# Kernel optimization log

Hardware: AMD Instinct MI355X
Metric: run time of the kernel (lower is better)

The kernel has to match this reference:

```python
import jax, jax.numpy as jnp
import numpy as np

N_NODES = 50000
N_EDGES = 600000
D_IN = 128
D_HID = 128
N_CLASS = 40


def gcn_conv(x, edge_index, W, b, num_nodes):
    """PyG GCNConv: add self-loops, symmetric normalization, weight-then-propagate."""
    row, col = edge_index[0], edge_index[1]
    loop = jnp.arange(num_nodes)
    row = jnp.concatenate([row, loop])
    col = jnp.concatenate([col, loop])
    ew = jnp.ones(row.shape[0], dtype=x.dtype)
    deg = jax.ops.segment_sum(ew, col, num_segments=num_nodes)  # in-degree incl. self-loop
    dinv = jnp.where(deg > 0, jax.lax.rsqrt(deg), jnp.zeros((), x.dtype))
    norm = dinv[row] * dinv[col]  # [E+N]
    xw = x @ W  # [N, D]
    msg = norm[:, None] * xw[row]  # gather + scale, [E+N, D]
    out = jax.ops.segment_sum(msg, col, num_segments=num_nodes)  # scatter-add
    return out + b


def setup_inputs() -> dict:
    key = jax.random.key(0)
    ks = jax.random.split(key, 8)
    s_in = 1.0 / np.sqrt(D_IN)
    s_hid = 1.0 / np.sqrt(D_HID)
    return {
        "x": jax.random.normal(ks[0], (N_NODES, D_IN), jnp.float32),
        "edge_index": jax.random.randint(ks[1], (2, N_EDGES), 0, N_NODES, dtype=jnp.int64),
        "W_in": jax.random.normal(ks[2], (D_IN, D_HID), jnp.float32) * s_in,
        "b_in": jnp.zeros((D_HID,), jnp.float32),
        "W_gcn": jax.random.normal(ks[3], (D_HID, D_HID), jnp.float32) * s_hid,
        "b_gcn": jnp.zeros((D_HID,), jnp.float32),
        "W_cls": jax.random.normal(ks[4], (D_HID, N_CLASS), jnp.float32) * s_hid,
        "b_cls": jnp.zeros((N_CLASS,), jnp.float32),
    }


def reference(x, edge_index, W_in, b_in, W_gcn, b_gcn, W_cls, b_cls):
    h = jax.nn.relu(x @ W_in + b_in)               # linear_transform_in
    g = gcn_conv(h, edge_index, W_gcn, b_gcn, N_NODES)  # GCNConv
    y_hat = jax.nn.relu(g) @ W_cls + b_cls          # linear_cls_out
    return y_hat
```

## Files before the change

### kernel.cpp

```cpp
#include <hip/hip_runtime.h>


typedef __bf16 bf16x8 __attribute__((ext_vector_type(8)));
typedef float f32x4 __attribute__((ext_vector_type(4)));

#define NBUCK 512
#define CH_MAX 4704
#define PREP_BLKS 76
#define SCAP 1024

__device__ __forceinline__ ushort f2b(float f) {
  uint u = __float_as_uint(f);
  return (ushort)((u + 0x7FFFu + ((u >> 16) & 1u)) >> 16);
}
__device__ __forceinline__ float b2f_lo(uint u) { return __uint_as_float(u << 16); }
__device__ __forceinline__ float b2f_hi(uint u) { return __uint_as_float(u & 0xFFFF0000u); }

__device__ __forceinline__ void acc8s(float* a, uint4 v, float d) {
  a[0] = fmaf(d, b2f_lo(v.x), a[0]); a[1] = fmaf(d, b2f_hi(v.x), a[1]);
  a[2] = fmaf(d, b2f_lo(v.y), a[2]); a[3] = fmaf(d, b2f_hi(v.y), a[3]);
  a[4] = fmaf(d, b2f_lo(v.z), a[4]); a[5] = fmaf(d, b2f_hi(v.z), a[5]);
  a[6] = fmaf(d, b2f_lo(v.w), a[6]); a[7] = fmaf(d, b2f_hi(v.w), a[7]);
}

template<bool ABF16, bool RELU, bool BIAS>
__device__ __forceinline__ void gemm_tile_512(const void* __restrict__ Ap,
                                              const ushort* __restrict__ Wt,
                                              const float* __restrict__ bias,
                                              ushort* __restrict__ O,
                                              int nrows, int row0,
                                              char* smem, int tid) {
  ushort (*As)[136] = (ushort(*)[136])smem;
  ushort (*Bs)[136] = (ushort(*)[136])(smem + 128 * 136 * 2);
#pragma unroll
  for (int q = 0; q < 4; ++q) {
    int f = tid + 512 * q;
    int r = f >> 4, cw = f & 15;
    *(uint4*)&Bs[r][cw * 8] = *(const uint4*)&Wt[r * 128 + cw * 8];
  }
  if (ABF16) {
    const ushort* A = (const ushort*)Ap;
#pragma unroll
    for (int q = 0; q < 4; ++q) {
      int f = tid + 512 * q;
      int r = f >> 4, cw = f & 15;
      uint4 v = make_uint4(0u, 0u, 0u, 0u);
      if (row0 + r < nrows) v = *(const uint4*)&A[(size_t)(row0 + r) * 128 + cw * 8];
      *(uint4*)&As[r][cw * 8] = v;
    }
  } else {
    const float* A = (const float*)Ap;
#pragma unroll
    for (int q = 0; q < 8; ++q) {
      int f = tid + 512 * q;
      int r = f >> 5, kc = f & 31;
      float4 v = make_float4(0.f, 0.f, 0.f, 0.f);
      if (row0 + r < nrows) v = *(const float4*)&A[(size_t)(row0 + r) * 128 + kc * 4];
      ushort4 o;
      o.x = f2b(v.x); o.y = f2b(v.y); o.z = f2b(v.z); o.w = f2b(v.w);
      *(ushort4*)&As[r][kc * 4] = o;
    }
  }
  __syncthreads();

  const int wid = tid >> 6, lane = tid & 63;
  const int fr = lane & 15, fg = lane >> 4;
  f32x4 acc[8];
#pragma unroll
  for (int nn = 0; nn < 8; ++nn) acc[nn] = (f32x4){0.f, 0.f, 0.f, 0.f};
#pragma unroll
  for (int ks = 0; ks < 4; ++ks) {
    const int kb = ks * 32 + fg * 8;
    bf16x8 a = *(const bf16x8*)&As[wid * 16 + fr][kb];
#pragma unroll
    for (int nn = 0; nn < 8; ++nn) {
      bf16x8 b = *(const bf16x8*)&Bs[nn * 16 + fr][kb];
      acc[nn] = __builtin_amdgcn_mfma_f32_16x16x32_bf16(a, b, acc[nn], 0, 0, 0);
    }
  }
  const int r0 = row0 + wid * 16 + fg * 4;
#pragma unroll
  for (int nn = 0; nn < 8; ++nn) {
    const int cn = nn * 16 + fr;
    const float bv = BIAS ? bias[cn] : 0.f;
#pragma unroll
    for (int i = 0; i < 4; ++i) {
      const int rr = r0 + i;
      if (rr < nrows) {
        float v = acc[nn][i] + bv;
        if (RELU) v = fmaxf(v, 0.f);
        O[(size_t)rr * 128 + cn] = f2b(v);
      }
    }
  }
}

__global__ __launch_bounds__(512) void k_L1_prep_chist(const float* __restrict__ Wi,
                                                       const float* __restrict__ Wg,
                                                       const float* __restrict__ Wc,
                                                       ushort* __restrict__ Ti,
                                                       ushort* __restrict__ Tg,
                                                       ushort* __restrict__ Tc,
                                                       const int* __restrict__ col,
                                                       int* __restrict__ H2,
                                                       int E, int chunk, int sortb) {
  __shared__ int hist[NBUCK];
  const int tid = threadIdx.x;
  if (blockIdx.x < PREP_BLKS) {
    int idx = blockIdx.x * 512 + tid;
    if (idx < 16384) {
      int c = idx >> 7, k = idx & 127;
      Ti[c * 128 + k] = f2b(Wi[k * 128 + c]);
    } else if (idx < 32768) {
      int j = idx - 16384;
      int c = j >> 7, k = j & 127;
      Tg[c * 128 + k] = f2b(Wg[k * 128 + c]);
    } else if (idx < 38912) {
      int j = idx - 32768;
      int c = j >> 7, k = j & 127;
      Tc[c * 128 + k] = (c < 40) ? f2b(Wc[k * 40 + c]) : (ushort)0;
    }
    return;
  }
  const int blk = blockIdx.x - PREP_BLKS;
  if (tid < NBUCK) hist[tid] = 0;
  __syncthreads();
  const int e0 = blk * chunk;
  const int cnt = min(chunk, E - e0);
  for (int i = tid; i < cnt; i += 512)
    atomicAdd(&hist[((unsigned)col[e0 + i]) >> 7], 1);
  __syncthreads();
  if (tid < NBUCK) H2[tid * sortb + blk] = hist[tid];
}

__global__ __launch_bounds__(512) void k_L2_scan_g1a(const int* __restrict__ H2,
                                                     int* __restrict__ Hs,
                                                     int* __restrict__ cursor,
                                                     int sortb,
                                                     const float* __restrict__ x,
                                                     const ushort* __restrict__ Wti,
                                                     const float* __restrict__ b_in,
                                                     ushort* __restrict__ h, int nrows) {
  __shared__ __align__(16) char smem[69632];
  const int tid = threadIdx.x;
  if (blockIdx.x == 0) {
    int* sd = (int*)smem;
    int s = 0;
    const int4* p = (const int4*)&H2[tid * sortb];
    for (int j = 0; j < sortb / 4; ++j) { int4 v = p[j]; s += v.x + v.y + v.z + v.w; }
    sd[tid] = s;
    __syncthreads();
    for (int off = 1; off < 512; off <<= 1) {
      int u = (tid >= off) ? sd[tid - off] : 0;
      __syncthreads();
      sd[tid] += u;
      __syncthreads();
    }
    Hs[tid] = sd[tid] - s;
    if (tid == 511) Hs[NBUCK] = sd[511];
    cursor[tid] = 0;
    return;
  }
  gemm_tile_512<false, true, true>(x, Wti, b_in, h, nrows,
                                   (blockIdx.x - 1) * 128, smem, tid);
}

__global__ __launch_bounds__(512) void k_L3_reorder_g1b_g2a(const int* __restrict__ row,
                                                            const int* __restrict__ col,
                                                            const int* __restrict__ Hs,
                                                            int* __restrict__ cursor,
                                                            uint* __restrict__ ebuf,
                                                            int E, int chunk, int sortb,
                                                            const float* __restrict__ x,
                                                            const ushort* __restrict__ Wti,
                                                            const float* __restrict__ b_in,
                                                            const ushort* __restrict__ Wtg,
                                                            ushort* __restrict__ h,
                                                            ushort* __restrict__ xws,
                                                            int nrows) {
  __shared__ __align__(16) char smem[69632];
  const int tid = threadIdx.x;
  const int NT = (nrows + 127) >> 7;
  const int SPLIT = (NT + 1) >> 1;
  if (blockIdx.x < (unsigned)sortb) {
    int* hist   = (int*)smem;
    int* lstart = hist + NBUCK;
    int* cnt2   = lstart + NBUCK;
    int* obase  = cnt2 + NBUCK;
    uint* data  = (uint*)(obase + NBUCK);
    int* gpos   = (int*)(data + CH_MAX);
    int* sd     = gpos + CH_MAX;
    hist[tid] = 0; cnt2[tid] = 0;
    __syncthreads();
    const int e0 = blockIdx.x * chunk;
    const int cnt = min(chunk, E - e0);
    for (int i = tid; i < cnt; i += 512)
      atomicAdd(&hist[((unsigned)col[e0 + i]) >> 7], 1);
    __syncthreads();
    const int h0 = hist[tid];
    sd[tid] = h0;
    __syncthreads();
    for (int off = 1; off < 512; off <<= 1) {
      int u = (tid >= off) ? sd[tid - off] : 0;
      __syncthreads();
      sd[tid] += u;
      __syncthreads();
    }
    lstart[tid] = sd[tid] - h0;
    obase[tid] = Hs[tid] + (h0 ? atomicAdd(&cursor[tid], h0) : 0);
    __syncthreads();
    for (int i = tid; i < cnt; i += 512) {
      const int c = col[e0 + i], r = row[e0 + i];
      const int b = ((unsigned)c) >> 7;
      const int rk = atomicAdd(&cnt2[b], 1);
      const int slot = lstart[b] + rk;
      data[slot] = ((uint)(c & 127) << 16) | (uint)r;
      gpos[slot] = obase[b] + rk;
    }
    __syncthreads();
    for (int i = tid; i < cnt; i += 512)
      ebuf[gpos[i]] = data[i];
    return;
  }
  const int t = blockIdx.x - sortb;
  if (t < NT - SPLIT) {
    gemm_tile_512<false, true, true>(x, Wti, b_in, h, nrows,
                                     (SPLIT + t) * 128, smem, tid);
  } else {
    gemm_tile_512<true, false, false>(h, Wtg, nullptr, xws, nrows,
                                      (t - (NT - SPLIT)) * 128, smem, tid);
  }
}

__global__ __launch_bounds__(512) void k_L4_sort_g2b(const uint* __restrict__ ebuf,
                                                     const int* __restrict__ Hs,
                                                     int* __restrict__ srcrow,
                                                     int* __restrict__ P,
                                                     float* __restrict__ dinv,
                                                     int nbuck,
                                                     const ushort* __restrict__ h,
                                                     const ushort* __restrict__ Wtg,
                                                     ushort* __restrict__ xws,
                                                     int n) {
  __shared__ __align__(16) char smem[69632];
  const int tid = threadIdx.x;
  if (blockIdx.x < (unsigned)nbuck) {
    int* cnt    = (int*)smem;
    int* lstart = cnt + 128;
    int* cnt2   = lstart + 128;
    int* sd     = cnt2 + 128;
    if (tid < 128) { cnt[tid] = 0; cnt2[tid] = 0; }
    __syncthreads();
    const int b = blockIdx.x;
    const int start = Hs[b];
    const int end = Hs[b + 1];
    for (int i = start + tid; i < end; i += 512)
      atomicAdd(&cnt[ebuf[i] >> 16], 1);
    __syncthreads();
    const int cv = (tid < 128) ? cnt[tid] : 0;
    sd[tid] = cv;
    __syncthreads();
    for (int off = 1; off < 128; off <<= 1) {
      int u = (tid >= off) ? sd[tid - off] : 0;
      __syncthreads();
      sd[tid] += u;
      __syncthreads();
    }
    if (tid < 128) {
      const int ex = sd[tid] - cv;
      lstart[tid] = ex;
      const int node = b * 128 + tid;
      if (node < n) {
        P[node] = start + ex + cv;
        dinv[node] = rsqrtf((float)cv + 1.0f);
      }
    }
    __syncthreads();
    for (int i = start + tid; i < end; i += 512) {
      const uint v = ebuf[i];
      const int c = v >> 16;
      const int rk = atomicAdd(&cnt2[c], 1);
      srcrow[start + lstart[c] + rk] = (int)(v & 0xFFFFu);
    }
    return;
  }
  const int NT = (n + 127) >> 7;
  const int SPLIT = (NT + 1) >> 1;
  const int t = blockIdx.x - nbuck;
  gemm_tile_512<true, false, false>(h, Wtg, nullptr, xws, n,
                                    (SPLIT + t) * 128, smem, tid);
}

__global__ __launch_bounds__(512) void k_aggout(const int* __restrict__ P,
                                                const int* __restrict__ srcrow,
                                                const ushort* __restrict__ xws,
                                                const float* __restrict__ dinv,
                                                const float* __restrict__ b_gcn,
                                                const ushort* __restrict__ Wtc,
                                                const float* __restrict__ bc,
                                                float* __restrict__ out, int n) {
  __shared__ ushort ts[32][136];
  __shared__ ushort Bs[48][136];
  __shared__ int eLds[SCAP];
  __shared__ int pb[33];
  __shared__ int nextn;
  const int tid = threadIdx.x;
  const int row0 = blockIdx.x * 32;
#pragma unroll
  for (int q = 0; q < 2; ++q) {
    int f = tid + 512 * q;
    if (f < 768) {
      int r = f >> 4, cw = f & 15;
      *(uint4*)&Bs[r][cw * 8] = *(const uint4*)&Wtc[r * 128 + cw * 8];
    }
  }
  if (tid < 33) {
    int node = row0 + tid - 1;
    pb[tid] = (node < 0) ? 0 : P[node < n ? node : (n - 1)];
  }
  if (tid == 0) nextn = 0;
  __syncthreads();
  const int sStart = pb[0];
  const int tot = pb[32] - sStart;
  const bool inL = (tot <= SCAP);
  if (inL) {
    for (int i = tid; i < tot; i += 512) eLds[i] = srcrow[sStart + i];
  }
  __syncthreads();

  const int wid = tid >> 6, lane = tid & 63;
  const int qt = lane >> 4, lq = lane & 15;
  const size_t coff = (size_t)lq * 8;

  float bg[8];
#pragma unroll
  for (int j = 0; j < 8; ++j) bg[j] = b_gcn[lq * 8 + j];

  for (;;) {
    int idx;
    if (lane == 0) idx = atomicAdd(&nextn, 1);
    idx = __shfl(idx, 0);
    if (idx >= 32) break;
    const int c = row0 + idx;
    if (c < n) {
      const int len = pb[idx + 1] - pb[idx];
      float a[8];
#pragma unroll
      for (int j = 0; j < 8; ++j) a[j] = 0.f;
      if (inL) {
        const int base = pb[idx] - sStart;
        int e = 0;
        for (; e + 8 <= len; e += 8) {
          const int r0 = eLds[base + e + qt];
          const int r1 = eLds[base + e + 4 + qt];
          const float d0 = dinv[r0], d1 = dinv[r1];
          const uint4 v0 = *(const uint4*)&xws[(size_t)r0 * 128 + coff];
          const uint4 v1 = *(const uint4*)&xws[(size_t)r1 * 128 + coff];
          acc8s(a, v0, d0);
          acc8s(a, v1, d1);
        }
        for (; e < len; e += 4) {
          if (e + qt < len) {
            const int r = eLds[base + e + qt];
            const float d = dinv[r];
            const uint4 v = *(const uint4*)&xws[(size_t)r * 128 + coff];
            acc8s(a, v, d);
          }
        }
      } else {
        const int base = pb[idx];
        int e = 0;
        for (; e + 8 <= len; e += 8) {
          const int r0 = srcrow[base + e + qt];
          const int r1 = srcrow[base + e + 4 + qt];
          const float d0 = dinv[r0], d1 = dinv[r1];
          const uint4 v0 = *(const uint4*)&xws[(size_t)r0 * 128 + coff];
          const uint4 v1 = *(const uint4*)&xws[(size_t)r1 * 128 + coff];
          acc8s(a, v0, d0);
          acc8s(a, v1, d1);
        }
        for (; e < len; e += 4) {
          if (e + qt < len) {
            const int r = srcrow[base + e + qt];
            const float d = dinv[r];
            const uint4 v = *(const uint4*)&xws[(size_t)r * 128 + coff];
            acc8s(a, v, d);
          }
        }
      }
#pragma unroll
      for (int j = 0; j < 8; ++j) {
        a[j] += __shfl_xor(a[j], 16);
        a[j] += __shfl_xor(a[j], 32);
      }
      if (qt == 0) {
        const uint4 sv = *(const uint4*)&xws[(size_t)c * 128 + coff];
        const float dc = dinv[c];
        acc8s(a, sv, dc);
        const float t0 = fmaxf(fmaf(dc, a[0], bg[0]), 0.f);
        const float t1 = fmaxf(fmaf(dc, a[1], bg[1]), 0.f);
        const float t2 = fmaxf(fmaf(dc, a[2], bg[2]), 0.f);
        const float t3 = fmaxf(fmaf(dc, a[3], bg[3]), 0.f);
        const float t4 = fmaxf(fmaf(dc, a[4], bg[4]), 0.f);
        const float t5 = fmaxf(fmaf(dc, a[5], bg[5]), 0.f);
        const float t6 = fmaxf(fmaf(dc, a[6], bg[6]), 0.f);
        const float t7 = fmaxf(fmaf(dc, a[7], bg[7]), 0.f);
        uint4 o;
        o.x = ((uint)f2b(t1) << 16) | f2b(t0);
        o.y = ((uint)f2b(t3) << 16) | f2b(t2);
        o.z = ((uint)f2b(t5) << 16) | f2b(t4);
        o.w = ((uint)f2b(t7) << 16) | f2b(t6);
        *(uint4*)&ts[idx][coff] = o;
      }
    } else if (qt == 0) {
      *(uint4*)&ts[idx][coff] = make_uint4(0u, 0u, 0u, 0u);
    }
  }
  __syncthreads();

  if (wid < 6) {
    const int rb = wid & 1, nb = wid >> 1;
    const int fr = lane & 15, fg = lane >> 4;
    f32x4 acc = (f32x4){0.f, 0.f, 0.f, 0.f};
#pragma unroll
    for (int ks = 0; ks < 4; ++ks) {
      const int kb = ks * 32 + fg * 8;
      bf16x8 aa = *(const bf16x8*)&ts[rb * 16 + fr][kb];
      bf16x8 bb = *(const bf16x8*)&Bs[nb * 16 + fr][kb];
      acc = __builtin_amdgcn_mfma_f32_16x16x32_bf16(aa, bb, acc, 0, 0, 0);
    }
    const int cn = nb * 16 + fr;
    if (cn < 40) {
      const float bv = bc[cn];
      const int r0 = row0 + rb * 16 + fg * 4;
#pragma unroll
      for (int i = 0; i < 4; ++i) {
        const int rr = r0 + i;
        if (rr < n) out[(size_t)rr * 40 + cn] = acc[i] + bv;
      }
    }
  }
}

extern "C" void kernel_launch(void* const* d_in, const int* in_sizes, int n_in,
                              void* d_out, int out_size, void* d_ws, size_t ws_size,
                              hipStream_t stream) {
  const float* x     = (const float*)d_in[0];
  const int*   ei    = (const int*)d_in[1];
  const float* W_in  = (const float*)d_in[2];
  const float* b_in  = (const float*)d_in[3];
  const float* W_gcn = (const float*)d_in[4];
  const float* b_gcn = (const float*)d_in[5];
  const float* W_cls = (const float*)d_in[6];
  const float* b_cls = (const float*)d_in[7];
  float* out = (float*)d_out;

  const int N = in_sizes[0] / 128;
  const int E = in_sizes[1] / 2;
  const int* row = ei;
  const int* col = ei + E;

  const int sortb = (E + CH_MAX - 1) / CH_MAX;
  const int chunk = (E + sortb - 1) / sortb;
  const int nbuck = (N + 127) >> 7;
  const int NT    = (N + 127) >> 7;
  const int SPLIT = (NT + 1) >> 1;

  ushort* h      = (ushort*)d_ws;
  ushort* xws    = h + (size_t)N * 128;
  ushort* Wti    = xws + (size_t)N * 128;
  ushort* Wtg    = Wti + 128 * 128;
  ushort* Wtc    = Wtg + 128 * 128;
  uint*   ebuf   = (uint*)(Wtc + 48 * 128);
  int*    srcrow = (int*)(ebuf + E);
  int*    H2     = srcrow + E;
  int*    Hs     = H2 + NBUCK * sortb;
  int*    cursor = Hs + NBUCK + 1;
  int*    P      = cursor + NBUCK;
  float*  dinv   = (float*)(P + N);

  k_L1_prep_chist<<<PREP_BLKS + sortb, 512, 0, stream>>>(
      W_in, W_gcn, W_cls, Wti, Wtg, Wtc, col, H2, E, chunk, sortb);

  k_L2_scan_g1a<<<1 + SPLIT, 512, 0, stream>>>(
      H2, Hs, cursor, sortb, x, Wti, b_in, h, N);

  k_L3_reorder_g1b_g2a<<<sortb + (NT - SPLIT) + SPLIT, 512, 0, stream>>>(
      row, col, Hs, cursor, ebuf, E, chunk, sortb,
      x, Wti, b_in, Wtg, h, xws, N);

  k_L4_sort_g2b<<<nbuck + (NT - SPLIT), 512, 0, stream>>>(
      ebuf, Hs, srcrow, P, dinv, nbuck, h, Wtg, xws, N);

  k_aggout<<<(N + 31) / 32, 512, 0, stream>>>(
      P, srcrow, xws, dinv, b_gcn, Wtc, b_cls, out, N);
}
```

Baseline: 79.64 us.

## Fuse input linear and GCN weight GEMMs per tile, rebalance across kernels

```diff
diff --git a/kernel.cpp b/kernel.cpp
--- a/kernel.cpp
+++ b/kernel.cpp
@@ -23,43 +23,30 @@
   a[6] = fmaf(d, b2f_lo(v.w), a[6]); a[7] = fmaf(d, b2f_hi(v.w), a[7]);
 }
 
-template<bool ABF16, bool RELU, bool BIAS>
-__device__ __forceinline__ void gemm_tile_512(const void* __restrict__ Ap,
-                                              const ushort* __restrict__ Wt,
-                                              const float* __restrict__ bias,
-                                              ushort* __restrict__ O,
-                                              int nrows, int row0,
-                                              char* smem, int tid) {
+__device__ __forceinline__ void g12_tile_512(const float* __restrict__ x,
+                                             const ushort* __restrict__ Wti,
+                                             const ushort* __restrict__ Wtg,
+                                             const float* __restrict__ b_in,
+                                             ushort* __restrict__ xws,
+                                             int nrows, int row0,
+                                             char* smem, int tid) {
   ushort (*As)[136] = (ushort(*)[136])smem;
   ushort (*Bs)[136] = (ushort(*)[136])(smem + 128 * 136 * 2);
 #pragma unroll
   for (int q = 0; q < 4; ++q) {
     int f = tid + 512 * q;
     int r = f >> 4, cw = f & 15;
-    *(uint4*)&Bs[r][cw * 8] = *(const uint4*)&Wt[r * 128 + cw * 8];
-  }
-  if (ABF16) {
-    const ushort* A = (const ushort*)Ap;
-#pragma unroll
-    for (int q = 0; q < 4; ++q) {
-      int f = tid + 512 * q;
-      int r = f >> 4, cw = f & 15;
-      uint4 v = make_uint4(0u, 0u, 0u, 0u);
-      if (row0 + r < nrows) v = *(const uint4*)&A[(size_t)(row0 + r) * 128 + cw * 8];
-      *(uint4*)&As[r][cw * 8] = v;
-    }
-  } else {
-    const float* A = (const float*)Ap;
-#pragma unroll
-    for (int q = 0; q < 8; ++q) {
-      int f = tid + 512 * q;
-      int r = f >> 5, kc = f & 31;
-      float4 v = make_float4(0.f, 0.f, 0.f, 0.f);
-      if (row0 + r < nrows) v = *(const float4*)&A[(size_t)(row0 + r) * 128 + kc * 4];
-      ushort4 o;
-      o.x = f2b(v.x); o.y = f2b(v.y); o.z = f2b(v.z); o.w = f2b(v.w);
-      *(ushort4*)&As[r][kc * 4] = o;
-    }
+    *(uint4*)&Bs[r][cw * 8] = *(const uint4*)&Wti[r * 128 + cw * 8];
+  }
+#pragma unroll
+  for (int q = 0; q < 8; ++q) {
+    int f = tid + 512 * q;
+    int r = f >> 5, kc = f & 31;
+    float4 v = make_float4(0.f, 0.f, 0.f, 0.f);
+    if (row0 + r < nrows) v = *(const float4*)&x[(size_t)(row0 + r) * 128 + kc * 4];
+    ushort4 o;
+    o.x = f2b(v.x); o.y = f2b(v.y); o.z = f2b(v.z); o.w = f2b(v.w);
+    *(ushort4*)&As[r][kc * 4] = o;
   }
   __syncthreads();
 
@@ -78,19 +65,45 @@
       acc[nn] = __builtin_amdgcn_mfma_f32_16x16x32_bf16(a, b, acc[nn], 0, 0, 0);
     }
   }
-  const int r0 = row0 + wid * 16 + fg * 4;
+  __syncthreads();
+
 #pragma unroll
   for (int nn = 0; nn < 8; ++nn) {
     const int cn = nn * 16 + fr;
-    const float bv = BIAS ? bias[cn] : 0.f;
+    const float bv = b_in[cn];
+#pragma unroll
+    for (int i = 0; i < 4; ++i)
+      As[wid * 16 + fg * 4 + i][cn] = f2b(fmaxf(acc[nn][i] + bv, 0.f));
+  }
+#pragma unroll
+  for (int q = 0; q < 4; ++q) {
+    int f = tid + 512 * q;
+    int r = f >> 4, cw = f & 15;
+    *(uint4*)&Bs[r][cw * 8] = *(const uint4*)&Wtg[r * 128 + cw * 8];
+  }
+  __syncthreads();
+
+  f32x4 acc2[8];
+#pragma unroll
+  for (int nn = 0; nn < 8; ++nn) acc2[nn] = (f32x4){0.f, 0.f, 0.f, 0.f};
+#pragma unroll
+  for (int ks = 0; ks < 4; ++ks) {
+    const int kb = ks * 32 + fg * 8;
+    bf16x8 a = *(const bf16x8*)&As[wid * 16 + fr][kb];
+#pragma unroll
+    for (int nn = 0; nn < 8; ++nn) {
+      bf16x8 b = *(const bf16x8*)&Bs[nn * 16 + fr][kb];
+      acc2[nn] = __builtin_amdgcn_mfma_f32_16x16x32_bf16(a, b, acc2[nn], 0, 0, 0);
+    }
+  }
+  const int r0 = row0 + wid * 16 + fg * 4;
+#pragma unroll
+  for (int nn = 0; nn < 8; ++nn) {
+    const int cn = nn * 16 + fr;
 #pragma unroll
     for (int i = 0; i < 4; ++i) {
       const int rr = r0 + i;
-      if (rr < nrows) {
-        float v = acc[nn][i] + bv;
-        if (RELU) v = fmaxf(v, 0.f);
-        O[(size_t)rr * 128 + cn] = f2b(v);
-      }
+      if (rr < nrows) xws[(size_t)rr * 128 + cn] = f2b(acc2[nn][i]);
     }
   }
 }
@@ -133,14 +146,16 @@
   if (tid < NBUCK) H2[tid * sortb + blk] = hist[tid];
 }
 
-__global__ __launch_bounds__(512) void k_L2_scan_g1a(const int* __restrict__ H2,
+__global__ __launch_bounds__(512) void k_L2_scan_g12(const int* __restrict__ H2,
                                                      int* __restrict__ Hs,
                                                      int* __restrict__ cursor,
                                                      int sortb,
                                                      const float* __restrict__ x,
                                                      const ushort* __restrict__ Wti,
+                                                     const ushort* __restrict__ Wtg,
                                                      const float* __restrict__ b_in,
-                                                     ushort* __restrict__ h, int nrows) {
+                                                     ushort* __restrict__ xws,
+                                                     int nrows) {
   __shared__ __align__(16) char smem[69632];
   const int tid = threadIdx.x;
   if (blockIdx.x == 0) {
@@ -161,27 +176,23 @@
     cursor[tid] = 0;
     return;
   }
-  gemm_tile_512<false, true, true>(x, Wti, b_in, h, nrows,
-                                   (blockIdx.x - 1) * 128, smem, tid);
-}
-
-__global__ __launch_bounds__(512) void k_L3_reorder_g1b_g2a(const int* __restrict__ row,
-                                                            const int* __restrict__ col,
-                                                            const int* __restrict__ Hs,
-                                                            int* __restrict__ cursor,
-                                                            uint* __restrict__ ebuf,
-                                                            int E, int chunk, int sortb,
-                                                            const float* __restrict__ x,
-                                                            const ushort* __restrict__ Wti,
-                                                            const float* __restrict__ b_in,
-                                                            const ushort* __restrict__ Wtg,
-                                                            ushort* __restrict__ h,
-                                                            ushort* __restrict__ xws,
-                                                            int nrows) {
+  g12_tile_512(x, Wti, Wtg, b_in, xws, nrows, (blockIdx.x - 1) * 128, smem, tid);
+}
+
+__global__ __launch_bounds__(512) void k_L3_reorder_g12(const int* __restrict__ row,
+                                                        const int* __restrict__ col,
+                                                        const int* __restrict__ Hs,
+                                                        int* __restrict__ cursor,
+                                                        uint* __restrict__ ebuf,
+                                                        int E, int chunk, int sortb,
+                                                        const float* __restrict__ x,
+                                                        const ushort* __restrict__ Wti,
+                                                        const ushort* __restrict__ Wtg,
+                                                        const float* __restrict__ b_in,
+                                                        ushort* __restrict__ xws,
+                                                        int nrows, int tile0) {
   __shared__ __align__(16) char smem[69632];
   const int tid = threadIdx.x;
-  const int NT = (nrows + 127) >> 7;
-  const int SPLIT = (NT + 1) >> 1;
   if (blockIdx.x < (unsigned)sortb) {
     int* hist   = (int*)smem;
     int* lstart = hist + NBUCK;
@@ -222,26 +233,22 @@
       ebuf[gpos[i]] = data[i];
     return;
   }
-  const int t = blockIdx.x - sortb;
-  if (t < NT - SPLIT) {
-    gemm_tile_512<false, true, true>(x, Wti, b_in, h, nrows,
-                                     (SPLIT + t) * 128, smem, tid);
-  } else {
-    gemm_tile_512<true, false, false>(h, Wtg, nullptr, xws, nrows,
-                                      (t - (NT - SPLIT)) * 128, smem, tid);
-  }
-}
-
-__global__ __launch_bounds__(512) void k_L4_sort_g2b(const uint* __restrict__ ebuf,
+  g12_tile_512(x, Wti, Wtg, b_in, xws, nrows,
+               (tile0 + (int)blockIdx.x - sortb) * 128, smem, tid);
+}
+
+__global__ __launch_bounds__(512) void k_L4_sort_g12(const uint* __restrict__ ebuf,
                                                      const int* __restrict__ Hs,
                                                      int* __restrict__ srcrow,
                                                      int* __restrict__ P,
                                                      float* __restrict__ dinv,
                                                      int nbuck,
-                                                     const ushort* __restrict__ h,
+                                                     const float* __restrict__ x,
+                                                     const ushort* __restrict__ Wti,
                                                      const ushort* __restrict__ Wtg,
+                                                     const float* __restrict__ b_in,
                                                      ushort* __restrict__ xws,
-                                                     int n) {
+                                                     int n, int tile0) {
   __shared__ __align__(16) char smem[69632];
   const int tid = threadIdx.x;
   if (blockIdx.x < (unsigned)nbuck) {
@@ -284,11 +291,8 @@
     }
     return;
   }
-  const int NT = (n + 127) >> 7;
-  const int SPLIT = (NT + 1) >> 1;
-  const int t = blockIdx.x - nbuck;
-  gemm_tile_512<true, false, false>(h, Wtg, nullptr, xws, n,
-                                    (SPLIT + t) * 128, smem, tid);
+  g12_tile_512(x, Wti, Wtg, b_in, xws, n,
+               (tile0 + (int)blockIdx.x - nbuck) * 128, smem, tid);
 }
 
 __global__ __launch_bounds__(512) void k_aggout(const int* __restrict__ P,
@@ -329,7 +333,7 @@
   __syncthreads();
 
   const int wid = tid >> 6, lane = tid & 63;
-  const int qt = lane >> 4, lq = lane & 15;
+  const int lq = lane & 15;
   const size_t coff = (size_t)lq * 8;
 
   float bg[8];
@@ -338,8 +342,8 @@
 
   for (;;) {
     int idx;
-    if (lane == 0) idx = atomicAdd(&nextn, 1);
-    idx = __shfl(idx, 0);
+    if (lq == 0) idx = atomicAdd(&nextn, 1);
+    idx = __shfl(idx, lane & 48);
     if (idx >= 32) break;
     const int c = row0 + idx;
     if (c < n) {
@@ -350,69 +354,56 @@
       if (inL) {
         const int base = pb[idx] - sStart;
         int e = 0;
-        for (; e + 8 <= len; e += 8) {
-          const int r0 = eLds[base + e + qt];
-          const int r1 = eLds[base + e + 4 + qt];
+        for (; e + 2 <= len; e += 2) {
+          const int r0 = eLds[base + e], r1 = eLds[base + e + 1];
           const float d0 = dinv[r0], d1 = dinv[r1];
           const uint4 v0 = *(const uint4*)&xws[(size_t)r0 * 128 + coff];
           const uint4 v1 = *(const uint4*)&xws[(size_t)r1 * 128 + coff];
           acc8s(a, v0, d0);
           acc8s(a, v1, d1);
         }
-        for (; e < len; e += 4) {
-          if (e + qt < len) {
-            const int r = eLds[base + e + qt];
-            const float d = dinv[r];
-            const uint4 v = *(const uint4*)&xws[(size_t)r * 128 + coff];
-            acc8s(a, v, d);
-          }
+        if (e < len) {
+          const int r = eLds[base + e];
+          const float d = dinv[r];
+          const uint4 v = *(const uint4*)&xws[(size_t)r * 128 + coff];
+          acc8s(a, v, d);
         }
       } else {
         const int base = pb[idx];
         int e = 0;
-        for (; e + 8 <= len; e += 8) {
-          const int r0 = srcrow[base + e + qt];
-          const int r1 = srcrow[base + e + 4 + qt];
+        for (; e + 2 <= len; e += 2) {
+          const int r0 = srcrow[base + e], r1 = srcrow[base + e + 1];
           const float d0 = dinv[r0], d1 = dinv[r1];
           const uint4 v0 = *(const uint4*)&xws[(size_t)r0 * 128 + coff];
           const uint4 v1 = *(const uint4*)&xws[(size_t)r1 * 128 + coff];
           acc8s(a, v0, d0);
           acc8s(a, v1, d1);
         }
-        for (; e < len; e += 4) {
-          if (e + qt < len) {
-            const int r = srcrow[base + e + qt];
-            const float d = dinv[r];
-            const uint4 v = *(const uint4*)&xws[(size_t)r * 128 + coff];
-            acc8s(a, v, d);
-          }
+        if (e < len) {
+          const int r = srcrow[base + e];
+          const float d = dinv[r];
+          const uint4 v = *(const uint4*)&xws[(size_t)r * 128 + coff];
+          acc8s(a, v, d);
         }
       }
-#pragma unroll
-      for (int j = 0; j < 8; ++j) {
-        a[j] += __shfl_xor(a[j], 16);
-        a[j] += __shfl_xor(a[j], 32);
-      }
-      if (qt == 0) {
-        const uint4 sv = *(const uint4*)&xws[(size_t)c * 128 + coff];
-        const float dc = dinv[c];
-        acc8s(a, sv, dc);
-        const float t0 = fmaxf(fmaf(dc, a[0], bg[0]), 0.f);
-        const float t1 = fmaxf(fmaf(dc, a[1], bg[1]), 0.f);
-        const float t2 = fmaxf(fmaf(dc, a[2], bg[2]), 0.f);
-        const float t3 = fmaxf(fmaf(dc, a[3], bg[3]), 0.f);
-        const float t4 = fmaxf(fmaf(dc, a[4], bg[4]), 0.f);
-        const float t5 = fmaxf(fmaf(dc, a[5], bg[5]), 0.f);
-        const float t6 = fmaxf(fmaf(dc, a[6], bg[6]), 0.f);
-        const float t7 = fmaxf(fmaf(dc, a[7], bg[7]), 0.f);
-        uint4 o;
-        o.x = ((uint)f2b(t1) << 16) | f2b(t0);
-        o.y = ((uint)f2b(t3) << 16) | f2b(t2);
-        o.z = ((uint)f2b(t5) << 16) | f2b(t4);
-        o.w = ((uint)f2b(t7) << 16) | f2b(t6);
-        *(uint4*)&ts[idx][coff] = o;
-      }
-    } else if (qt == 0) {
+      const uint4 sv = *(const uint4*)&xws[(size_t)c * 128 + coff];
+      const float dc = dinv[c];
+      acc8s(a, sv, dc);
+      const float t0 = fmaxf(fmaf(dc, a[0], bg[0]), 0.f);
+      const float t1 = fmaxf(fmaf(dc, a[1], bg[1]), 0.f);
+      const float t2 = fmaxf(fmaf(dc, a[2], bg[2]), 0.f);
+      const float t3 = fmaxf(fmaf(dc, a[3], bg[3]), 0.f);
+      const float t4 = fmaxf(fmaf(dc, a[4], bg[4]), 0.f);
+      const float t5 = fmaxf(fmaf(dc, a[5], bg[5]), 0.f);
+      const float t6 = fmaxf(fmaf(dc, a[6], bg[6]), 0.f);
+      const float t7 = fmaxf(fmaf(dc, a[7], bg[7]), 0.f);
+      uint4 o;
+      o.x = ((uint)f2b(t1) << 16) | f2b(t0);
+      o.y = ((uint)f2b(t3) << 16) | f2b(t2);
+      o.z = ((uint)f2b(t5) << 16) | f2b(t4);
+      o.w = ((uint)f2b(t7) << 16) | f2b(t6);
+      *(uint4*)&ts[idx][coff] = o;
+    } else {
       *(uint4*)&ts[idx][coff] = make_uint4(0u, 0u, 0u, 0u);
     }
   }
@@ -464,10 +455,10 @@
   const int chunk = (E + sortb - 1) / sortb;
   const int nbuck = (N + 127) >> 7;
   const int NT    = (N + 127) >> 7;
-  const int SPLIT = (NT + 1) >> 1;
-
-  ushort* h      = (ushort*)d_ws;
-  ushort* xws    = h + (size_t)N * 128;
+  const int T1    = NT / 3;
+  const int T2    = (2 * NT) / 3;
+
+  ushort* xws    = (ushort*)d_ws;
   ushort* Wti    = xws + (size_t)N * 128;
   ushort* Wtg    = Wti + 128 * 128;
   ushort* Wtc    = Wtg + 128 * 128;
@@ -482,15 +473,15 @@
   k_L1_prep_chist<<<PREP_BLKS + sortb, 512, 0, stream>>>(
       W_in, W_gcn, W_cls, Wti, Wtg, Wtc, col, H2, E, chunk, sortb);
 
-  k_L2_scan_g1a<<<1 + SPLIT, 512, 0, stream>>>(
-      H2, Hs, cursor, sortb, x, Wti, b_in, h, N);
-
-  k_L3_reorder_g1b_g2a<<<sortb + (NT - SPLIT) + SPLIT, 512, 0, stream>>>(
+  k_L2_scan_g12<<<1 + T1, 512, 0, stream>>>(
+      H2, Hs, cursor, sortb, x, Wti, Wtg, b_in, xws, N);
+
+  k_L3_reorder_g12<<<sortb + (T2 - T1), 512, 0, stream>>>(
       row, col, Hs, cursor, ebuf, E, chunk, sortb,
-      x, Wti, b_in, Wtg, h, xws, N);
-
-  k_L4_sort_g2b<<<nbuck + (NT - SPLIT), 512, 0, stream>>>(
-      ebuf, Hs, srcrow, P, dinv, nbuck, h, Wtg, xws, N);
+      x, Wti, Wtg, b_in, xws, N, T1);
+
+  k_L4_sort_g12<<<nbuck + (NT - T2), 512, 0, stream>>>(
+      ebuf, Hs, srcrow, P, dinv, nbuck, x, Wti, Wtg, b_in, xws, N, T2);
 
   k_aggout<<<(N + 31) / 32, 512, 0, stream>>>(
       P, srcrow, xws, dinv, b_gcn, Wtc, b_cls, out, N);
```

Result: faster. 77.41 us (median of 2 runs) (-2.8%).
